# Kernel optimization log

Measured on AMD Instinct MI355X. Metric: run time of the kernel, lower is better.

Reference implementation:

```python
import jax, jax.numpy as jnp
import numpy as np

B, N, E, D = 256, 1000, 16000, 32
NUM_ITEMS = 30
# TopKPooling ratio=0.8: k = ceil(0.8 * n_prev), static per layer
K1, K2, K3 = 800, 640, 512


def setup_inputs() -> dict:
    key = jax.random.key(0)
    ks = jax.random.split(key, 24)
    def gp(k, shape, s=0.1):
        return jax.random.normal(k, shape, dtype=jnp.float32) * s
    return dict(
        x_ids=jax.random.randint(ks[0], (B, N), 0, NUM_ITEMS + 1),
        edge_index=jax.random.randint(ks[1], (B, 2, E), 0, N, dtype=jnp.int32),
        emb=gp(ks[2], (NUM_ITEMS + 1, D), 1.0),
        w1=gp(ks[3], (D, D)), b1=gp(ks[4], (D,)), u1=gp(ks[5], (D, 2 * D)), p1=gp(ks[6], (D,), 1.0),
        w2=gp(ks[7], (D, D)), b2=gp(ks[8], (D,)), u2=gp(ks[9], (D, 2 * D)), p2=gp(ks[10], (D,), 1.0),
        w3=gp(ks[11], (D, D)), b3=gp(ks[12], (D,)), u3=gp(ks[13], (D, 2 * D)), p3=gp(ks[14], (D,), 1.0),
        l1w=gp(ks[15], (D, 2 * D)), l1b=gp(ks[16], (D,)),
        l2w=gp(ks[17], (D // 2, D)), l2b=gp(ks[18], (D // 2,)),
        l3w=gp(ks[19], (1, D // 2)), l3b=gp(ks[20], (1,)),
    )


def reference(x_ids, edge_index, emb, w1, b1, u1, p1, w2, b2, u2, p2,
              w3, b3, u3, p3, l1w, l1b, l2w, l2b, l3w, l3b):
    def sage(x, src, dst, emask, W, b, U):
        n = x.shape[0]
        h = jax.nn.relu(x @ W.T + b)                      # per-node msg (lin applied per edge == per node then gather)
        dst2 = jnp.where(emask, dst, n)                    # route invalid edges to dummy segment
        aggr = jax.ops.segment_max(h[src], dst2, num_segments=n + 1)[:n]
        aggr = jnp.maximum(aggr, h)                        # add_self_loops under max-aggr; also fixes empty segments
        return jax.nn.relu(jnp.concatenate([aggr, x], axis=-1) @ U.T)

    def pool(x, src, dst, emask, p, k):
        n = x.shape[0]
        score = jnp.tanh(x @ p / jnp.linalg.norm(p))
        vals, perm = jax.lax.top_k(score, k)
        xn = x[perm] * vals[:, None]
        newidx = jnp.full((n,), -1, jnp.int32).at[perm].set(jnp.arange(k, dtype=jnp.int32))
        s2, d2 = newidx[src], newidx[dst]
        valid = emask & (s2 >= 0) & (d2 >= 0)
        return xn, jnp.where(valid, s2, 0), jnp.where(valid, d2, 0), valid

    def per_graph(ids, ei):
        x = emb[ids]                                       # [N, D]
        src, dst = ei[0], ei[1]
        emask = jnp.ones((E,), bool)
        x = sage(x, src, dst, emask, w1, b1, u1)
        x, src, dst, emask = pool(x, src, dst, emask, p1, K1)
        r1 = jnp.concatenate([x.max(0), x.mean(0)])        # gmp || gap -> [2D]
        x = sage(x, src, dst, emask, w2, b2, u2)
        x, src, dst, emask = pool(x, src, dst, emask, p2, K2)
        r2 = jnp.concatenate([x.max(0), x.mean(0)])
        x = sage(x, src, dst, emask, w3, b3, u3)
        x, src, dst, emask = pool(x, src, dst, emask, p3, K3)
        r3 = jnp.concatenate([x.max(0), x.mean(0)])
        e = r1 + r2 + r3
        h = jax.nn.relu(e @ l1w.T + l1b)
        h = jax.nn.relu(h @ l2w.T + l2b)                   # dropout inactive (eval mode)
        o = jax.nn.sigmoid(h @ l3w.T + l3b)
        return o[0], e

    out, embed = jax.vmap(per_graph)(x_ids, edge_index)
    return out, embed
```

## Files before the change

kernel.cpp:

```cpp
#include <hip/hip_runtime.h>

#define NGRAPH 256
#define NNODE  1000
#define NEDGE  16000
#define DIM    32
#define HSTR   20

__device__ __forceinline__ unsigned monof(float f) {
  unsigned b = __float_as_uint(f);
  return (b & 0x80000000u) ? ~b : (b | 0x80000000u);
}

__device__ __forceinline__ float4 f4max(float4 a, float4 b) {
  return make_float4(fmaxf(a.x,b.x), fmaxf(a.y,b.y), fmaxf(a.z,b.z), fmaxf(a.w,b.w));
}
__device__ __forceinline__ float4 f4relu(float4 a) {
  return make_float4(fmaxf(a.x,0.f), fmaxf(a.y,0.f), fmaxf(a.z,0.f), fmaxf(a.w,0.f));
}
__device__ __forceinline__ float4 f4scale(float4 a, float s) {
  return make_float4(a.x*s, a.y*s, a.z*s, a.w*s);
}
__device__ __forceinline__ float4 f4add(float4 a, float4 b) {
  return make_float4(a.x+b.x, a.y+b.y, a.z+b.z, a.w+b.w);
}
__device__ __forceinline__ float dot4(float4 a, float4 b) {
  return a.x*b.x + a.y*b.y + a.z*b.z + a.w*b.w;
}
__device__ __forceinline__ float4 shfl4(float4 v, int m) {
  return make_float4(__shfl_xor(v.x,m,64), __shfl_xor(v.y,m,64),
                     __shfl_xor(v.z,m,64), __shfl_xor(v.w,m,64));
}
__device__ __forceinline__ float4 lds4(const float* p) { return *(const float4*)p; }

struct __align__(16) Smem {
  union { float h[NNODE * HSTR]; unsigned stage[NEDGE]; } hu;
  unsigned short csr[NEDGE];
  unsigned rowStart[1004];
  unsigned cnt[1024];
  unsigned histA[257];
  unsigned histB[257];
  unsigned wsum[16];
  float redm[512];
  float reds[512];
  float eacc[64];
  float hbuf[48];
  unsigned char alv[1024];
};

__device__ __forceinline__ unsigned blockExclScan(unsigned v, unsigned* wsum, int tid) {
  __syncthreads();
  int lane = tid & 63, w = tid >> 6;
  unsigned x = v;
  #pragma unroll
  for (int d = 1; d < 64; d <<= 1) {
    unsigned t = __shfl_up(x, d, 64);
    if (lane >= d) x += t;
  }
  if (lane == 63) wsum[w] = x;
  __syncthreads();
  if (w == 0) {
    unsigned s = (lane < 16) ? wsum[lane] : 0u;
    #pragma unroll
    for (int d = 1; d < 16; d <<= 1) {
      unsigned t = __shfl_up(s, d, 64);
      if (lane >= d) s += t;
    }
    if (lane < 16) wsum[lane] = s;
  }
  __syncthreads();
  unsigned base = (w > 0) ? wsum[w - 1] : 0u;
  return base + x - v;
}

#define XDOT(P4, R, S, O) ( dot4((P4)[(R)*(S)+(O)  ], x0) + dot4((P4)[(R)*(S)+(O)+1], x1) \
                          + dot4((P4)[(R)*(S)+(O)+2], x2) + dot4((P4)[(R)*(S)+(O)+3], x3) \
                          + dot4((P4)[(R)*(S)+(O)+4], x4) + dot4((P4)[(R)*(S)+(O)+5], x5) \
                          + dot4((P4)[(R)*(S)+(O)+6], x6) + dot4((P4)[(R)*(S)+(O)+7], x7) )
#define GDOT(R, O) ( dot4(U4[(R)*16+(O)  ], h0) + dot4(U4[(R)*16+(O)+1], h1) \
                   + dot4(U4[(R)*16+(O)+2], h2) + dot4(U4[(R)*16+(O)+3], h3) )
#define ACC4(v, R)    v.x  = XDOT(U4,(R),16,8); v.y  = XDOT(U4,(R)+1,16,8); v.z  = XDOT(U4,(R)+2,16,8); v.w  = XDOT(U4,(R)+3,16,8);
#define ACC4ADD(v, R, O) v.x += GDOT((R),(O)); v.y += GDOT((R)+1,(O)); v.z += GDOT((R)+2,(O)); v.w += GDOT((R)+3,(O));
#define HV4(v, R)     v.x = fmaxf(Bv[(R)]+XDOT(W4,(R),8,0),0.f); v.y = fmaxf(Bv[(R)+1]+XDOT(W4,(R)+1,8,0),0.f); \
                      v.z = fmaxf(Bv[(R)+2]+XDOT(W4,(R)+2,8,0),0.f); v.w = fmaxf(Bv[(R)+3]+XDOT(W4,(R)+3,8,0),0.f);
#define REDCH(v, OFF) do { \
  float4 mx = act ? (v) : make_float4(-__builtin_inff(),-__builtin_inff(),-__builtin_inff(),-__builtin_inff()); \
  float4 sv = act ? (v) : make_float4(0.f,0.f,0.f,0.f); \
  mx = f4max(mx, shfl4(mx,32)); sv = f4add(sv, shfl4(sv,32)); \
  mx = f4max(mx, shfl4(mx,16)); sv = f4add(sv, shfl4(sv,16)); \
  mx = f4max(mx, shfl4(mx, 8)); sv = f4add(sv, shfl4(sv, 8)); \
  mx = f4max(mx, shfl4(mx, 4)); sv = f4add(sv, shfl4(sv, 4)); \
  mx = f4max(mx, shfl4(mx, 2)); sv = f4add(sv, shfl4(sv, 2)); \
  mx = f4max(mx, shfl4(mx, 1)); sv = f4add(sv, shfl4(sv, 1)); \
  if (lane == 0) { *((float4*)(sm.redm + wv*32 + (OFF))) = mx; *((float4*)(sm.reds + wv*32 + (OFF))) = sv; } \
} while (0)

extern "C" __global__ void
__attribute__((amdgpu_flat_work_group_size(1024,1024)))
__attribute__((amdgpu_waves_per_eu(4,4)))
gnn_topk_kernel(const int* __restrict__ x_ids, const int* __restrict__ eidx,
                const float* __restrict__ emb,
                const float* __restrict__ w1, const float* __restrict__ b1,
                const float* __restrict__ u1, const float* __restrict__ p1,
                const float* __restrict__ w2, const float* __restrict__ b2,
                const float* __restrict__ u2, const float* __restrict__ p2,
                const float* __restrict__ w3, const float* __restrict__ b3,
                const float* __restrict__ u3, const float* __restrict__ p3,
                const float* __restrict__ l1w, const float* __restrict__ l1b,
                const float* __restrict__ l2w, const float* __restrict__ l2b,
                const float* __restrict__ l3w, const float* __restrict__ l3b,
                float* __restrict__ out)
{
  const int g = blockIdx.x;
  const int tid = (int)threadIdx.x;
  const int lane = tid & 63, wv = tid >> 6;

  __shared__ Smem sm;
  float* h_lds = sm.hu.h;

  const int* esrc = eidx + (size_t)g * (2 * NEDGE);
  const int* edst = esrc + NEDGE;

  float4 x0,x1,x2,x3,x4,x5,x6,x7;
  bool alive = (tid < NNODE);
  if (alive) {
    int id = x_ids[(size_t)g * NNODE + tid];
    const float4* ep = (const float4*)(emb + id * DIM);
    x0=ep[0]; x1=ep[1]; x2=ep[2]; x3=ep[3]; x4=ep[4]; x5=ep[5]; x6=ep[6]; x7=ep[7];
  } else {
    x0=x1=x2=x3=x4=x5=x6=x7=make_float4(0.f,0.f,0.f,0.f);
  }
  sm.alv[tid] = alive ? 1 : 0;
  if (tid < 64) sm.eacc[tid] = 0.f;
  __syncthreads();

  #pragma unroll 1
  for (int layer = 0; layer < 3; ++layer) {
    const float* W  = (layer==0)? w1 : (layer==1)? w2 : w3;
    const float* Bv = (layer==0)? b1 : (layer==1)? b2 : b3;
    const float* U  = (layer==0)? u1 : (layer==1)? u2 : u3;
    const float* P  = (layer==0)? p1 : (layer==1)? p2 : p3;
    const int k     = (layer==0)? 800 : (layer==1)? 640 : 512;
    const float4* W4 = (const float4*)W;
    const float4* U4 = (const float4*)U;

    if (layer == 0) {
      sm.cnt[tid] = 0u;
      __syncthreads();
      for (int e = tid; e < NEDGE; e += 1024) {
        int s = esrc[e];
        int d = edst[e];
        atomicAdd(&sm.cnt[d], 1u);
        sm.hu.stage[e] = ((unsigned)d << 16) | (unsigned)s;
      }
      __syncthreads();
      unsigned cv = sm.cnt[tid];
      unsigned excl = blockExclScan(cv, sm.wsum, tid);
      unsigned total = sm.wsum[15];
      if (tid < NNODE) sm.rowStart[tid] = excl;
      if (tid == 0) sm.rowStart[NNODE] = total;
      sm.cnt[tid] = excl;
      __syncthreads();
      for (int e = tid; e < NEDGE; e += 1024) {
        unsigned pk = sm.hu.stage[e];
        unsigned d = pk >> 16;
        unsigned pos = atomicAdd(&sm.cnt[d], 1u);
        sm.csr[pos] = (unsigned short)(pk & 0xFFFFu);
      }
      __syncthreads();
    }

    unsigned wbeg = 0, wend = 0;
    if (tid < NNODE) { wbeg = sm.rowStart[tid]; wend = sm.rowStart[tid + 1]; }

    float4* hp = (float4*)(h_lds + tid * HSTR);

    float4 a0,a1,a2,a3,a4,a5,a6,a7;
    float4 h0,h1,h2,h3;
    if (alive) {
      ACC4(a0,0) ACC4(a1,4) ACC4(a2,8) ACC4(a3,12) ACC4(a4,16) ACC4(a5,20) ACC4(a6,24) ACC4(a7,28)
      HV4(h0,0) HV4(h1,4) HV4(h2,8) HV4(h3,12)
      hp[0]=h0; hp[1]=h1; hp[2]=h2; hp[3]=h3;
    }
    __syncthreads();
    if (alive) {
      for (unsigned e = wbeg; e < wend; ++e) {
        int s = sm.csr[e];
        if (sm.alv[s]) {
          const float* rp = h_lds + s * HSTR;
          h0 = f4max(h0, lds4(rp));   h1 = f4max(h1, lds4(rp+4));
          h2 = f4max(h2, lds4(rp+8)); h3 = f4max(h3, lds4(rp+12));
        }
      }
      ACC4ADD(a0,0,0) ACC4ADD(a1,4,0) ACC4ADD(a2,8,0) ACC4ADD(a3,12,0)
      ACC4ADD(a4,16,0) ACC4ADD(a5,20,0) ACC4ADD(a6,24,0) ACC4ADD(a7,28,0)
    }
    __syncthreads();
    if (alive) {
      HV4(h0,16) HV4(h1,20) HV4(h2,24) HV4(h3,28)
      hp[0]=h0; hp[1]=h1; hp[2]=h2; hp[3]=h3;
    }
    __syncthreads();
    if (alive) {
      for (unsigned e = wbeg; e < wend; ++e) {
        int s = sm.csr[e];
        if (sm.alv[s]) {
          const float* rp = h_lds + s * HSTR;
          h0 = f4max(h0, lds4(rp));   h1 = f4max(h1, lds4(rp+4));
          h2 = f4max(h2, lds4(rp+8)); h3 = f4max(h3, lds4(rp+12));
        }
      }
      ACC4ADD(a0,0,4) ACC4ADD(a1,4,4) ACC4ADD(a2,8,4) ACC4ADD(a3,12,4)
      ACC4ADD(a4,16,4) ACC4ADD(a5,20,4) ACC4ADD(a6,24,4) ACC4ADD(a7,28,4)
      x0=f4relu(a0); x1=f4relu(a1); x2=f4relu(a2); x3=f4relu(a3);
      x4=f4relu(a4); x5=f4relu(a5); x6=f4relu(a6); x7=f4relu(a7);
    }

    float pn = 0.f;
    for (int c = 0; c < DIM; ++c) pn += P[c] * P[c];
    pn = sqrtf(pn);
    const float4* P4 = (const float4*)P;
    unsigned key = 0xFFFFFFFFu;
    float val = 0.f;
    if (alive) {
      float dp = dot4(P4[0],x0)+dot4(P4[1],x1)+dot4(P4[2],x2)+dot4(P4[3],x3)
               + dot4(P4[4],x4)+dot4(P4[5],x5)+dot4(P4[6],x6)+dot4(P4[7],x7);
      val = tanhf(dp / pn);
      key = ~monof(val);
    }
    for (int i = tid; i < 257; i += 1024) { sm.histA[i] = 0u; sm.histB[i] = 0u; }
    __syncthreads();

    if (alive) { hp[0]=x0; hp[1]=x1; hp[2]=x2; hp[3]=x3; }

    bool cand = alive;
    bool sel = false;
    unsigned target = (unsigned)k;
    unsigned dig = (key >> 24) & 255u;
    if (cand) atomicAdd(&sm.histA[dig], 1u);
    __syncthreads();
    #pragma unroll 1
    for (int p = 0; p < 4; ++p) {
      unsigned* buf  = (p & 1) ? sm.histB : sm.histA;
      unsigned* nbuf = (p & 1) ? sm.histA : sm.histB;
      if (tid < 64) {
        unsigned q0 = buf[tid*4], q1 = buf[tid*4+1], q2 = buf[tid*4+2], q3 = buf[tid*4+3];
        unsigned s1 = q0+q1, s2v = s1+q2, s3 = s2v+q3;
        unsigned tot = s3;
        #pragma unroll
        for (int d = 1; d < 64; d <<= 1) {
          unsigned t = __shfl_up(tot, d, 64);
          if (lane >= d) tot += t;
        }
        unsigned base = tot - s3;
        buf[tid*4] = base; buf[tid*4+1] = base+q0; buf[tid*4+2] = base+s1; buf[tid*4+3] = base+s2v;
        if (tid == 63) buf[256] = tot;
      } else if (p > 0 && p < 3) {
        for (int i = tid - 64; i < 257; i += 960) nbuf[i] = 0u;
      }
      __syncthreads();
      if (cand) {
        unsigned lo = buf[dig], hi = buf[dig+1];
        if (hi <= target)      { sel = true;  cand = false; }
        else if (lo >= target) { cand = false; }
        else                   { target -= lo; }
      }
      if (p < 3) {
        dig = (key >> (16 - 8*p)) & 255u;
        if (cand) atomicAdd(&nbuf[dig], 1u);
      }
      __syncthreads();
    }
    {
      unsigned long long bm = __ballot(cand);
      if (lane == 0) sm.wsum[wv] = (unsigned)__popcll(bm);
      __syncthreads();
      unsigned pre = 0;
      for (int w_ = 0; w_ < wv; ++w_) pre += sm.wsum[w_];
      unsigned trank = pre + (unsigned)__popcll(bm & ((1ULL << lane) - 1ULL));
      if (cand && trank < target) sel = true;
    }

    if (alive) { x0 = hp[0]; x1 = hp[1]; x2 = hp[2]; x3 = hp[3]; }
    alive = sel;
    sm.alv[tid] = sel ? 1 : 0;
    if (sel) {
      x0=f4scale(x0,val); x1=f4scale(x1,val); x2=f4scale(x2,val); x3=f4scale(x3,val);
      x4=f4scale(x4,val); x5=f4scale(x5,val); x6=f4scale(x6,val); x7=f4scale(x7,val);
    } else {
      x0=x1=x2=x3=x4=x5=x6=x7=make_float4(0.f,0.f,0.f,0.f);
    }

    {
      bool act = alive;
      REDCH(x0, 0); REDCH(x1, 4); REDCH(x2, 8);  REDCH(x3, 12);
      REDCH(x4,16); REDCH(x5,20); REDCH(x6,24);  REDCH(x7,28);
    }
    __syncthreads();
    if (tid < 32) {
      float rm = -__builtin_inff(), rs = 0.f;
      #pragma unroll
      for (int w_ = 0; w_ < 16; ++w_) {
        rm = fmaxf(rm, sm.redm[w_*32 + tid]);
        rs += sm.reds[w_*32 + tid];
      }
      sm.eacc[tid] += rm;
      sm.eacc[32 + tid] += rs / (float)k;
    }
    __syncthreads();
  }

  if (tid < 32) {
    float v = l1b[tid];
    #pragma unroll
    for (int c = 0; c < 64; ++c) v += l1w[tid*64 + c] * sm.eacc[c];
    sm.hbuf[tid] = fmaxf(v, 0.f);
  }
  __syncthreads();
  if (tid < 16) {
    float v = l2b[tid];
    #pragma unroll
    for (int c = 0; c < 32; ++c) v += l2w[tid*32 + c] * sm.hbuf[c];
    sm.hbuf[32 + tid] = fmaxf(v, 0.f);
  }
  __syncthreads();
  if (tid == 0) {
    float v = l3b[0];
    #pragma unroll
    for (int c = 0; c < 16; ++c) v += l3w[c] * sm.hbuf[32 + c];
    out[g] = 1.f / (1.f + expf(-v));
  }
  if (tid < 64) out[NGRAPH + (size_t)g*64 + tid] = sm.eacc[tid];
}

extern "C" void kernel_launch(void* const* d_in, const int* in_sizes, int n_in,
                              void* d_out, int out_size, void* d_ws, size_t ws_size,
                              hipStream_t stream) {
  (void)in_sizes; (void)n_in; (void)d_ws; (void)ws_size; (void)out_size;
  const int*   x_ids = (const int*)d_in[0];
  const int*   eidx  = (const int*)d_in[1];
  const float* emb   = (const float*)d_in[2];
  const float* w1 = (const float*)d_in[3],  *b1 = (const float*)d_in[4];
  const float* u1 = (const float*)d_in[5],  *p1 = (const float*)d_in[6];
  const float* w2 = (const float*)d_in[7],  *b2 = (const float*)d_in[8];
  const float* u2 = (const float*)d_in[9],  *p2 = (const float*)d_in[10];
  const float* w3 = (const float*)d_in[11], *b3 = (const float*)d_in[12];
  const float* u3 = (const float*)d_in[13], *p3 = (const float*)d_in[14];
  const float* l1w = (const float*)d_in[15], *l1b = (const float*)d_in[16];
  const float* l2w = (const float*)d_in[17], *l2b = (const float*)d_in[18];
  const float* l3w = (const float*)d_in[19], *l3b = (const float*)d_in[20];
  float* out = (float*)d_out;

  gnn_topk_kernel<<<dim3(NGRAPH), dim3(1024), 0, stream>>>(
      x_ids, eidx, emb,
      w1, b1, u1, p1, w2, b2, u2, p2, w3, b3, u3, p3,
      l1w, l1b, l2w, l2b, l3w, l3b, out);
}
```

Measured before the change: 260.8 us.

## Store full 32-wide messages in LDS and move CSR adjacency to global workspace

```diff
diff --git a/kernel.cpp b/kernel.cpp
--- a/kernel.cpp
+++ b/kernel.cpp
@@ -4,7 +4,7 @@
 #define NNODE  1000
 #define NEDGE  16000
 #define DIM    32
-#define HSTR   20
+#define HSTR   36
 
 __device__ __forceinline__ unsigned monof(float f) {
   unsigned b = __float_as_uint(f);
@@ -34,7 +34,6 @@
 
 struct __align__(16) Smem {
   union { float h[NNODE * HSTR]; unsigned stage[NEDGE]; } hu;
-  unsigned short csr[NEDGE];
   unsigned rowStart[1004];
   unsigned cnt[1024];
   unsigned histA[257];
@@ -108,6 +107,7 @@
                 const float* __restrict__ l1w, const float* __restrict__ l1b,
                 const float* __restrict__ l2w, const float* __restrict__ l2b,
                 const float* __restrict__ l3w, const float* __restrict__ l3b,
+                unsigned short* __restrict__ gcsr_all,
                 float* __restrict__ out)
 {
   const int g = blockIdx.x;
@@ -116,6 +116,7 @@
 
   __shared__ Smem sm;
   float* h_lds = sm.hu.h;
+  unsigned short* gcsr = gcsr_all + (size_t)g * NEDGE;
 
   const int* esrc = eidx + (size_t)g * (2 * NEDGE);
   const int* edst = esrc + NEDGE;
@@ -164,7 +165,7 @@
         unsigned pk = sm.hu.stage[e];
         unsigned d = pk >> 16;
         unsigned pos = atomicAdd(&sm.cnt[d], 1u);
-        sm.csr[pos] = (unsigned short)(pk & 0xFFFFu);
+        gcsr[pos] = (unsigned short)(pk & 0xFFFFu);
       }
       __syncthreads();
     }
@@ -175,16 +176,22 @@
     float4* hp = (float4*)(h_lds + tid * HSTR);
 
     float4 a0,a1,a2,a3,a4,a5,a6,a7;
+    if (alive) {
+      float4 t;
+      HV4(t,0)  hp[0]=t;  HV4(t,4)  hp[1]=t;
+      HV4(t,8)  hp[2]=t;  HV4(t,12) hp[3]=t;
+      HV4(t,16) hp[4]=t;  HV4(t,20) hp[5]=t;
+      HV4(t,24) hp[6]=t;  HV4(t,28) hp[7]=t;
+      ACC4(a0,0) ACC4(a1,4) ACC4(a2,8) ACC4(a3,12)
+      ACC4(a4,16) ACC4(a5,20) ACC4(a6,24) ACC4(a7,28)
+    }
+    __syncthreads();
+
     float4 h0,h1,h2,h3;
     if (alive) {
-      ACC4(a0,0) ACC4(a1,4) ACC4(a2,8) ACC4(a3,12) ACC4(a4,16) ACC4(a5,20) ACC4(a6,24) ACC4(a7,28)
-      HV4(h0,0) HV4(h1,4) HV4(h2,8) HV4(h3,12)
-      hp[0]=h0; hp[1]=h1; hp[2]=h2; hp[3]=h3;
-    }
-    __syncthreads();
-    if (alive) {
+      h0 = hp[0]; h1 = hp[1]; h2 = hp[2]; h3 = hp[3];
       for (unsigned e = wbeg; e < wend; ++e) {
-        int s = sm.csr[e];
+        int s = gcsr[e];
         if (sm.alv[s]) {
           const float* rp = h_lds + s * HSTR;
           h0 = f4max(h0, lds4(rp));   h1 = f4max(h1, lds4(rp+4));
@@ -194,17 +201,12 @@
       ACC4ADD(a0,0,0) ACC4ADD(a1,4,0) ACC4ADD(a2,8,0) ACC4ADD(a3,12,0)
       ACC4ADD(a4,16,0) ACC4ADD(a5,20,0) ACC4ADD(a6,24,0) ACC4ADD(a7,28,0)
     }
-    __syncthreads();
     if (alive) {
-      HV4(h0,16) HV4(h1,20) HV4(h2,24) HV4(h3,28)
-      hp[0]=h0; hp[1]=h1; hp[2]=h2; hp[3]=h3;
-    }
-    __syncthreads();
-    if (alive) {
+      h0 = hp[4]; h1 = hp[5]; h2 = hp[6]; h3 = hp[7];
       for (unsigned e = wbeg; e < wend; ++e) {
-        int s = sm.csr[e];
+        int s = gcsr[e];
         if (sm.alv[s]) {
-          const float* rp = h_lds + s * HSTR;
+          const float* rp = h_lds + s * HSTR + 16;
           h0 = f4max(h0, lds4(rp));   h1 = f4max(h1, lds4(rp+4));
           h2 = f4max(h2, lds4(rp+8)); h3 = f4max(h3, lds4(rp+12));
         }
@@ -229,8 +231,6 @@
     }
     for (int i = tid; i < 257; i += 1024) { sm.histA[i] = 0u; sm.histB[i] = 0u; }
     __syncthreads();
-
-    if (alive) { hp[0]=x0; hp[1]=x1; hp[2]=x2; hp[3]=x3; }
 
     bool cand = alive;
     bool sel = false;
@@ -280,7 +280,6 @@
       if (cand && trank < target) sel = true;
     }
 
-    if (alive) { x0 = hp[0]; x1 = hp[1]; x2 = hp[2]; x3 = hp[3]; }
     alive = sel;
     sm.alv[tid] = sel ? 1 : 0;
     if (sel) {
@@ -335,7 +334,7 @@
 extern "C" void kernel_launch(void* const* d_in, const int* in_sizes, int n_in,
                               void* d_out, int out_size, void* d_ws, size_t ws_size,
                               hipStream_t stream) {
-  (void)in_sizes; (void)n_in; (void)d_ws; (void)ws_size; (void)out_size;
+  (void)in_sizes; (void)n_in; (void)ws_size; (void)out_size;
   const int*   x_ids = (const int*)d_in[0];
   const int*   eidx  = (const int*)d_in[1];
   const float* emb   = (const float*)d_in[2];
@@ -349,9 +348,10 @@
   const float* l2w = (const float*)d_in[17], *l2b = (const float*)d_in[18];
   const float* l3w = (const float*)d_in[19], *l3b = (const float*)d_in[20];
   float* out = (float*)d_out;
+  unsigned short* gcsr = (unsigned short*)d_ws;
 
   gnn_topk_kernel<<<dim3(NGRAPH), dim3(1024), 0, stream>>>(
       x_ids, eidx, emb,
       w1, b1, u1, p1, w2, b2, u2, p2, w3, b3, u3, p3,
-      l1w, l1b, l2w, l2b, l3w, l3b, out);
-}
+      l1w, l1b, l2w, l2b, l3w, l3b, gcsr, out);
+}
```

New measurement: 272.2 us. 4.3% more time.

## Store SAGE messages as bf16 in LDS and aggregate all channels in one pass

Applied to the files above, without the earlier changes.

```diff
diff --git a/kernel.cpp b/kernel.cpp
--- a/kernel.cpp
+++ b/kernel.cpp
@@ -4,7 +4,7 @@
 #define NNODE  1000
 #define NEDGE  16000
 #define DIM    32
-#define HSTR   20
+#define HSU    40
 
 __device__ __forceinline__ unsigned monof(float f) {
   unsigned b = __float_as_uint(f);
@@ -30,10 +30,9 @@
   return make_float4(__shfl_xor(v.x,m,64), __shfl_xor(v.y,m,64),
                      __shfl_xor(v.z,m,64), __shfl_xor(v.w,m,64));
 }
-__device__ __forceinline__ float4 lds4(const float* p) { return *(const float4*)p; }
 
 struct __align__(16) Smem {
-  union { float h[NNODE * HSTR]; unsigned stage[NEDGE]; } hu;
+  union { unsigned short h[NNODE * HSU]; unsigned stage[NEDGE]; } hu;
   unsigned short csr[NEDGE];
   unsigned rowStart[1004];
   unsigned cnt[1024];
@@ -44,7 +43,6 @@
   float reds[512];
   float eacc[64];
   float hbuf[48];
-  unsigned char alv[1024];
 };
 
 __device__ __forceinline__ unsigned blockExclScan(unsigned v, unsigned* wsum, int tid) {
@@ -71,6 +69,14 @@
   unsigned base = (w > 0) ? wsum[w - 1] : 0u;
   return base + x - v;
 }
+
+#define CVTB(d, lo, hi) asm("v_cvt_pk_bf16_f32 %0, %1, %2" : "=v"(d) : "v"(lo), "v"(hi))
+#define CVTQ(q, t0, t1) CVTB(q.x,t0.x,t0.y); CVTB(q.y,t0.z,t0.w); CVTB(q.z,t1.x,t1.y); CVTB(q.w,t1.z,t1.w)
+#define PKM(a, b) asm("v_pk_max_u16 %0, %0, %1" : "+v"(a) : "v"(b))
+#define XLO(u) __uint_as_float((u) << 16)
+#define XHI(u) __uint_as_float((u) & 0xFFFF0000u)
+#define EXPAND(ha, hb_, gq) ha = make_float4(XLO((gq).x),XHI((gq).x),XLO((gq).y),XHI((gq).y)); \
+                            hb_ = make_float4(XLO((gq).z),XHI((gq).z),XLO((gq).w),XHI((gq).w))
 
 #define XDOT(P4, R, S, O) ( dot4((P4)[(R)*(S)+(O)  ], x0) + dot4((P4)[(R)*(S)+(O)+1], x1) \
                           + dot4((P4)[(R)*(S)+(O)+2], x2) + dot4((P4)[(R)*(S)+(O)+3], x3) \
@@ -115,7 +121,7 @@
   const int lane = tid & 63, wv = tid >> 6;
 
   __shared__ Smem sm;
-  float* h_lds = sm.hu.h;
+  unsigned short* hb = sm.hu.h;
 
   const int* esrc = eidx + (size_t)g * (2 * NEDGE);
   const int* edst = esrc + NEDGE;
@@ -129,7 +135,6 @@
   } else {
     x0=x1=x2=x3=x4=x5=x6=x7=make_float4(0.f,0.f,0.f,0.f);
   }
-  sm.alv[tid] = alive ? 1 : 0;
   if (tid < 64) sm.eacc[tid] = 0.f;
   __syncthreads();
 
@@ -172,43 +177,42 @@
     unsigned wbeg = 0, wend = 0;
     if (tid < NNODE) { wbeg = sm.rowStart[tid]; wend = sm.rowStart[tid + 1]; }
 
-    float4* hp = (float4*)(h_lds + tid * HSTR);
+    uint4* hq = (uint4*)(hb + tid * HSU);
 
     float4 a0,a1,a2,a3,a4,a5,a6,a7;
-    float4 h0,h1,h2,h3;
+    if (tid < NNODE) {
+      if (alive) {
+        float4 t0, t1; uint4 q;
+        HV4(t0,0)  HV4(t1,4)  CVTQ(q,t0,t1); hq[0]=q;
+        HV4(t0,8)  HV4(t1,12) CVTQ(q,t0,t1); hq[1]=q;
+        HV4(t0,16) HV4(t1,20) CVTQ(q,t0,t1); hq[2]=q;
+        HV4(t0,24) HV4(t1,28) CVTQ(q,t0,t1); hq[3]=q;
+      } else {
+        uint4 z = make_uint4(0,0,0,0);
+        hq[0]=z; hq[1]=z; hq[2]=z; hq[3]=z;
+      }
+    }
     if (alive) {
-      ACC4(a0,0) ACC4(a1,4) ACC4(a2,8) ACC4(a3,12) ACC4(a4,16) ACC4(a5,20) ACC4(a6,24) ACC4(a7,28)
-      HV4(h0,0) HV4(h1,4) HV4(h2,8) HV4(h3,12)
-      hp[0]=h0; hp[1]=h1; hp[2]=h2; hp[3]=h3;
-    }
-    __syncthreads();
+      ACC4(a0,0) ACC4(a1,4) ACC4(a2,8) ACC4(a3,12)
+      ACC4(a4,16) ACC4(a5,20) ACC4(a6,24) ACC4(a7,28)
+    }
+    __syncthreads();
+
     if (alive) {
+      uint4 g0 = hq[0], g1 = hq[1], g2 = hq[2], g3 = hq[3];
       for (unsigned e = wbeg; e < wend; ++e) {
-        int s = sm.csr[e];
-        if (sm.alv[s]) {
-          const float* rp = h_lds + s * HSTR;
-          h0 = f4max(h0, lds4(rp));   h1 = f4max(h1, lds4(rp+4));
-          h2 = f4max(h2, lds4(rp+8)); h3 = f4max(h3, lds4(rp+12));
-        }
-      }
+        const uint4* rp = (const uint4*)(hb + sm.csr[e] * HSU);
+        uint4 v0 = rp[0], v1 = rp[1], v2 = rp[2], v3 = rp[3];
+        PKM(g0.x,v0.x); PKM(g0.y,v0.y); PKM(g0.z,v0.z); PKM(g0.w,v0.w);
+        PKM(g1.x,v1.x); PKM(g1.y,v1.y); PKM(g1.z,v1.z); PKM(g1.w,v1.w);
+        PKM(g2.x,v2.x); PKM(g2.y,v2.y); PKM(g2.z,v2.z); PKM(g2.w,v2.w);
+        PKM(g3.x,v3.x); PKM(g3.y,v3.y); PKM(g3.z,v3.z); PKM(g3.w,v3.w);
+      }
+      float4 h0,h1,h2,h3;
+      EXPAND(h0,h1,g0); EXPAND(h2,h3,g1);
       ACC4ADD(a0,0,0) ACC4ADD(a1,4,0) ACC4ADD(a2,8,0) ACC4ADD(a3,12,0)
       ACC4ADD(a4,16,0) ACC4ADD(a5,20,0) ACC4ADD(a6,24,0) ACC4ADD(a7,28,0)
-    }
-    __syncthreads();
-    if (alive) {
-      HV4(h0,16) HV4(h1,20) HV4(h2,24) HV4(h3,28)
-      hp[0]=h0; hp[1]=h1; hp[2]=h2; hp[3]=h3;
-    }
-    __syncthreads();
-    if (alive) {
-      for (unsigned e = wbeg; e < wend; ++e) {
-        int s = sm.csr[e];
-        if (sm.alv[s]) {
-          const float* rp = h_lds + s * HSTR;
-          h0 = f4max(h0, lds4(rp));   h1 = f4max(h1, lds4(rp+4));
-          h2 = f4max(h2, lds4(rp+8)); h3 = f4max(h3, lds4(rp+12));
-        }
-      }
+      EXPAND(h0,h1,g2); EXPAND(h2,h3,g3);
       ACC4ADD(a0,0,4) ACC4ADD(a1,4,4) ACC4ADD(a2,8,4) ACC4ADD(a3,12,4)
       ACC4ADD(a4,16,4) ACC4ADD(a5,20,4) ACC4ADD(a6,24,4) ACC4ADD(a7,28,4)
       x0=f4relu(a0); x1=f4relu(a1); x2=f4relu(a2); x3=f4relu(a3);
@@ -229,8 +233,6 @@
     }
     for (int i = tid; i < 257; i += 1024) { sm.histA[i] = 0u; sm.histB[i] = 0u; }
     __syncthreads();
-
-    if (alive) { hp[0]=x0; hp[1]=x1; hp[2]=x2; hp[3]=x3; }
 
     bool cand = alive;
     bool sel = false;
@@ -280,9 +282,7 @@
       if (cand && trank < target) sel = true;
     }
 
-    if (alive) { x0 = hp[0]; x1 = hp[1]; x2 = hp[2]; x3 = hp[3]; }
     alive = sel;
-    sm.alv[tid] = sel ? 1 : 0;
     if (sel) {
       x0=f4scale(x0,val); x1=f4scale(x1,val); x2=f4scale(x2,val); x3=f4scale(x3,val);
       x4=f4scale(x4,val); x5=f4scale(x5,val); x6=f4scale(x6,val); x7=f4scale(x7,val);
```

New measurement: 217.5 us. 16.6% less time.
